# Performance work log

Hardware: AMD Instinct MI355X
Metric: run time of the kernel (lower is better)

The kernel has to match this reference:

```python
import jax, jax.numpy as jnp
import numpy as np

N_USERS, N_ITEMS = 100000, 50000
DIM = 128
E_U, E_I = 400000, 200000
B = 4096


def _init_layer(key, dim):
    k1, k2, k3 = jax.random.split(key, 3)
    s = 1.0 / np.sqrt(dim)
    W = jax.random.uniform(k1, (dim, dim), jnp.float32, -s, s)
    a_src = jax.random.uniform(k2, (dim,), jnp.float32, -s, s)
    a_dst = jax.random.uniform(k3, (dim,), jnp.float32, -s, s)
    return W, a_src, a_dst


def setup_inputs() -> dict:
    key = jax.random.key(0)
    ks = jax.random.split(key, 12)
    inp = {
        "uedg_index": jax.random.randint(ks[0], (2, E_U), 0, N_USERS),
        "iedg_index": jax.random.randint(ks[1], (2, E_I), 0, N_ITEMS),
        "user_id": jax.random.randint(ks[2], (B,), 0, N_USERS),
        "item_id": jax.random.randint(ks[3], (B,), 0, N_ITEMS),
        "uedg_value": jax.random.uniform(ks[4], (E_U,), jnp.float32),
        "iedg_value": jax.random.uniform(ks[5], (E_I,), jnp.float32),
        # learned parameters (t.rand init in the original)
        "user_matrix": jax.random.uniform(ks[6], (N_USERS, DIM), jnp.float32),
        "item_matrix": jax.random.uniform(ks[7], (N_ITEMS, DIM), jnp.float32),
    }
    for name, k in (("u1", ks[8]), ("u2", ks[9]), ("i1", ks[10]), ("i2", ks[11])):
        W, a_s, a_d = _init_layer(k, DIM)
        inp[f"W_{name}"] = W
        inp[f"a_src_{name}"] = a_s
        inp[f"a_dst_{name}"] = a_d
    return inp


def gat_layer(x, edge_index, edge_value, W, a_src, a_dst):
    """Single-head GAT layer with per-edge weights (dropout disabled / eval mode)."""
    n = x.shape[0]
    h = x @ W                                   # [N, D]
    src, dst = edge_index[0], edge_index[1]
    hs, hd = h[src], h[dst]                     # [E, D] gathers
    logits = jax.nn.leaky_relu((hs * a_src).sum(-1) + (hd * a_dst).sum(-1), 0.2)  # [E]
    # numerically-stable neighbor softmax over destination nodes
    m = jax.ops.segment_max(logits, dst, num_segments=n)
    e = jnp.exp(logits - m[dst]) * edge_value
    denom = jax.ops.segment_sum(e, dst, num_segments=n)
    coef = e / (denom[dst] + 1e-16)
    out = jax.ops.segment_sum(hs * coef[:, None], dst, num_segments=n)  # scatter-add aggregation
    return jax.nn.elu(out)


def reference(uedg_index, iedg_index, user_id, item_id, uedg_value, iedg_value,
              user_matrix, item_matrix,
              W_u1, a_src_u1, a_dst_u1, W_u2, a_src_u2, a_dst_u2,
              W_i1, a_src_i1, a_dst_i1, W_i2, a_src_i2, a_dst_i2):
    iout = gat_layer(item_matrix, iedg_index, iedg_value, W_i1, a_src_i1, a_dst_i1)
    uout = gat_layer(user_matrix, uedg_index, uedg_value, W_u1, a_src_u1, a_dst_u1)
    iout = gat_layer(iout, iedg_index, iedg_value, W_i2, a_src_i2, a_dst_i2)
    uout = gat_layer(uout, uedg_index, uedg_value, W_u2, a_src_u2, a_dst_u2)
    user_vc = uout[user_id]   # index_select over rows
    item_vc = iout[item_id]
    return user_vc, item_vc
```

## Files before the change

kernel.cpp:

```cpp
#include <hip/hip_runtime.h>
#include <hip/hip_bf16.h>

#define DIM 128
#define KSEG 32

typedef short bf16x8 __attribute__((ext_vector_type(8)));
typedef float f32x4  __attribute__((ext_vector_type(4)));

__device__ __forceinline__ float elu_f(float x) { return x > 0.f ? x : expm1f(x); }

__device__ __forceinline__ unsigned short f2bfu(float f) {
    return __builtin_bit_cast(unsigned short, __float2bfloat16(f));
}
__device__ __forceinline__ float bf2f(unsigned short b) {
    return __uint_as_float(((unsigned)b) << 16);
}

struct PrepArgs {
    const float* W[4];
    const float* as[4];
    const float* ad[4];
    unsigned short* Wt;
    unsigned short* wa;
};

__global__ __launch_bounds__(256) void init_all(int* __restrict__ z, int n, PrepArgs p, int nz)
{
    const int t = threadIdx.x;
    if ((int)blockIdx.x < nz) {
        int i = blockIdx.x * 256 + t;
        if (i < n) z[i] = 0;
        return;
    }
    __shared__ float as[DIM], ad[DIM];
    __shared__ float sr[4][2];
    const int pb    = blockIdx.x - nz;
    const int layer = pb >> 3;
    const int blk   = pb & 7;
    const float* W  = p.W[layer];
    unsigned short* W_t = p.Wt + layer * DIM * DIM;
    unsigned short* wa  = p.wa + layer * 2 * DIM;
    if (t < DIM) as[t] = p.as[layer][t];
    else ad[t - DIM] = p.ad[layer][t - DIM];
    __syncthreads();
    const int half = t >> 7;
    const int c = t & 127;
    const int wv = t >> 6;
    const int k_end = blk * 16 + 16;
    for (int k0 = blk * 16; k0 < k_end; k0 += 2) {
        const int k = k0 + half;
        float w = W[k * DIM + c];
        W_t[c * DIM + k] = f2bfu(w);
        float vs = w * as[c], vd = w * ad[c];
#pragma unroll
        for (int o = 32; o > 0; o >>= 1) { vs += __shfl_down(vs, o); vd += __shfl_down(vd, o); }
        if ((t & 63) == 0) { sr[wv][0] = vs; sr[wv][1] = vd; }
        __syncthreads();
        if (t < 2) {
            const int kk = k0 + t;
            wa[kk]       = f2bfu(sr[2 * t][0] + sr[2 * t + 1][0]);
            wa[DIM + kk] = f2bfu(sr[2 * t][1] + sr[2 * t + 1][1]);
        }
        __syncthreads();
    }
}

__global__ __launch_bounds__(256) void hist_gemm(
    const int* __restrict__ ued, const int* __restrict__ ied,
    const float* __restrict__ uval, const float* __restrict__ ival,
    int EU, int EI, int* __restrict__ cnt, int2* __restrict__ epair, int gH,
    const float* __restrict__ xu, const float* __restrict__ xi,
    const unsigned short* __restrict__ Wt_u, const unsigned short* __restrict__ Wt_i,
    const unsigned short* __restrict__ wa_u, const unsigned short* __restrict__ wa_i,
    unsigned short* __restrict__ h, float* __restrict__ s_src, float* __restrict__ s_dst,
    int NU, int NI, int gu)
{
    __shared__ short xs[2][64 * 128];
    const int t = threadIdx.x;

    if ((int)blockIdx.x < gH) {
        const int ET = EU + EI;
        const int stride = gH * 256;
        int e0 = blockIdx.x * 256 + t;
        int nd[4], sv[4]; float vv[4];
#pragma unroll
        for (int j = 0; j < 4; ++j) {
            int e = e0 + j * stride;
            nd[j] = -1;
            if (e < ET) {
                if (e < EU) { nd[j] = ued[EU + e]; sv[j] = ued[e]; vv[j] = uval[e]; }
                else { int ee = e - EU; nd[j] = NU + ied[EI + ee]; sv[j] = NU + ied[ee]; vv[j] = ival[ee]; }
            }
        }
        int rk[4];
#pragma unroll
        for (int j = 0; j < 4; ++j)
            if (nd[j] >= 0) rk[j] = atomicAdd(&cnt[nd[j]], 1);
#pragma unroll
        for (int j = 0; j < 4; ++j)
            if (nd[j] >= 0 && rk[j] < KSEG)
                epair[(size_t)nd[j] * KSEG + rk[j]] = make_int2(sv[j], __float_as_int(vv[j]));
        return;
    }

    const int wv = t >> 6;
    const int l  = t & 63;
    const int lo = l & 15;
    const int hi = l >> 4;

    const int gbid = blockIdx.x - gH;
    const bool isU = gbid < gu;
    const int b0   = isU ? gbid : gbid - gu;
    const int nblk = isU ? gu : (gridDim.x - gH - gu);
    const int Nl   = isU ? NU : NI;
    const int gofs = isU ? 0 : NU;
    const float* xf = isU ? xu : xi;
    const unsigned short* W_t = isU ? Wt_u : Wt_i;
    const unsigned short* wa  = isU ? wa_u : wa_i;
    const int ntiles = (Nl + 63) >> 6;
    if (b0 >= ntiles) return;

    bf16x8 wf[4][2];
#pragma unroll
    for (int cb2 = 0; cb2 < 2; ++cb2) {
        const unsigned short* base = W_t + (wv * 32 + cb2 * 16 + lo) * DIM + hi * 8;
#pragma unroll
        for (int kb = 0; kb < 4; ++kb)
            wf[kb][cb2] = *reinterpret_cast<const bf16x8*>(base + kb * 32);
    }
    bf16x8 sfrag[4];
    if (lo < 2) {
        const unsigned short* sb = wa + lo * DIM + hi * 8;
#pragma unroll
        for (int kb = 0; kb < 4; ++kb)
            sfrag[kb] = *reinterpret_cast<const bf16x8*>(sb + kb * 32);
    } else {
#pragma unroll
        for (int kb = 0; kb < 4; ++kb) {
            bf16x8 z = { 0, 0, 0, 0, 0, 0, 0, 0 };
            sfrag[kb] = z;
        }
    }

    int srow[4], suc[4];
#pragma unroll
    for (int i = 0; i < 4; ++i) {
        int unit = i * 256 + t;
        srow[i] = unit >> 4;
        suc[i]  = unit & 15;
    }
    float4 va[4], vb[4];

    auto LOADREGS = [&](int r0) {
#pragma unroll
        for (int i = 0; i < 4; ++i) {
            int gr = r0 + srow[i];
            if (gr < Nl) {
                const float4* p = reinterpret_cast<const float4*>(&xf[(size_t)gr * DIM + suc[i] * 8]);
                va[i] = p[0];
                vb[i] = p[1];
            } else {
                va[i] = make_float4(0.f, 0.f, 0.f, 0.f);
                vb[i] = make_float4(0.f, 0.f, 0.f, 0.f);
            }
        }
    };
    auto STORELDS = [&](int buf) {
#pragma unroll
        for (int i = 0; i < 4; ++i) {
            bf16x8 bv;
            bv[0] = (short)f2bfu(va[i].x); bv[1] = (short)f2bfu(va[i].y);
            bv[2] = (short)f2bfu(va[i].z); bv[3] = (short)f2bfu(va[i].w);
            bv[4] = (short)f2bfu(vb[i].x); bv[5] = (short)f2bfu(vb[i].y);
            bv[6] = (short)f2bfu(vb[i].z); bv[7] = (short)f2bfu(vb[i].w);
            int byte = srow[i] * 256 + ((suc[i] * 16) ^ ((srow[i] & 7) << 4));
            *reinterpret_cast<bf16x8*>(reinterpret_cast<char*>(xs[buf]) + byte) = bv;
        }
    };

    int tile = b0;
    LOADREGS(tile * 64);
    STORELDS(0);
    __syncthreads();
    int cur = 0;
    for (;;) {
        const int nextTile = tile + nblk;
        const bool more = nextTile < ntiles;
        if (more) LOADREGS(nextTile * 64);

        const int r0 = tile * 64;
#pragma unroll
        for (int rb = 0; rb < 4; ++rb) {
            const int arow = rb * 16 + lo;
            bf16x8 a[4];
#pragma unroll
            for (int kb = 0; kb < 4; ++kb) {
                int byte = arow * 256 + ((kb * 64 + hi * 16) ^ ((arow & 7) << 4));
                a[kb] = *reinterpret_cast<const bf16x8*>(reinterpret_cast<const char*>(xs[cur]) + byte);
            }
            f32x4 acc0 = {0.f,0.f,0.f,0.f}, acc1 = {0.f,0.f,0.f,0.f};
#pragma unroll
            for (int kb = 0; kb < 4; ++kb) {
                acc0 = __builtin_amdgcn_mfma_f32_16x16x32_bf16(a[kb], wf[kb][0], acc0, 0, 0, 0);
                acc1 = __builtin_amdgcn_mfma_f32_16x16x32_bf16(a[kb], wf[kb][1], acc1, 0, 0, 0);
            }
#pragma unroll
            for (int i = 0; i < 4; ++i) {
                int row = r0 + rb * 16 + hi * 4 + i;
                if (row < Nl) {
                    size_t grow = (size_t)(gofs + row);
                    h[grow * DIM + wv * 32 + lo]      = f2bfu(acc0[i]);
                    h[grow * DIM + wv * 32 + 16 + lo] = f2bfu(acc1[i]);
                }
            }
            if (rb == wv) {
                f32x4 acc_s = {0.f,0.f,0.f,0.f};
#pragma unroll
                for (int kb = 0; kb < 4; ++kb)
                    acc_s = __builtin_amdgcn_mfma_f32_16x16x32_bf16(a[kb], sfrag[kb], acc_s, 0, 0, 0);
#pragma unroll
                for (int i = 0; i < 4; ++i) {
                    int row = r0 + wv * 16 + hi * 4 + i;
                    if (row < Nl) {
                        if (lo == 0) s_src[gofs + row] = acc_s[i];
                        else if (lo == 1) s_dst[gofs + row] = acc_s[i];
                    }
                }
            }
        }

        if (!more) break;
        STORELDS(cur ^ 1);
        __syncthreads();
        cur ^= 1;
        tile = nextTile;
    }
}

__global__ __launch_bounds__(256) void mark_flag(const int* __restrict__ uid, const int* __restrict__ iid,
                                                 int B, int NU, const int* __restrict__ cnt,
                                                 const int2* __restrict__ epair, int* __restrict__ flag)
{
    int ent = (blockIdx.x * 256 + threadIdx.x) >> 4;
    int l16 = threadIdx.x & 15;
    if (ent >= 2 * B) return;
    int n = (ent < B) ? uid[ent] : NU + iid[ent - B];
    if (l16 == 0) flag[n] = 1;
    int md = min(cnt[n], KSEG);
    for (int e = l16; e < md; e += 16)
        flag[epair[(size_t)n * KSEG + e].x] = 1;
}

__global__ __launch_bounds__(256) void scan_partial(const int* __restrict__ cnt, int N, int* __restrict__ aux)
{
    __shared__ int sm[4];
    int i = blockIdx.x * 256 + threadIdx.x;
    int v = (i < N) ? cnt[i] : 0;
#pragma unroll
    for (int o = 32; o > 0; o >>= 1) v += __shfl_down(v, o);
    if ((threadIdx.x & 63) == 0) sm[threadIdx.x >> 6] = v;
    __syncthreads();
    if (threadIdx.x == 0) aux[blockIdx.x] = sm[0] + sm[1] + sm[2] + sm[3];
}

__global__ __launch_bounds__(1024) void scan_aux(int* __restrict__ aux, int nb)
{
    __shared__ int s[1024];
    int t = threadIdx.x;
    int v = (t < nb) ? aux[t] : 0;
    s[t] = v;
    __syncthreads();
    for (int o = 1; o < 1024; o <<= 1) {
        int u = (t >= o) ? s[t - o] : 0;
        __syncthreads();
        s[t] += u;
        __syncthreads();
    }
    if (t < nb) aux[t] = t ? s[t - 1] : 0;
}

__global__ __launch_bounds__(256) void scan_write(const int* __restrict__ cnt, const int* __restrict__ aux,
                                                  int N, int* __restrict__ rowptr)
{
    __shared__ int s[256];
    int t = threadIdx.x;
    int i = blockIdx.x * 256 + t;
    int v = (i < N) ? cnt[i] : 0;
    s[t] = v;
    __syncthreads();
    for (int o = 1; o < 256; o <<= 1) {
        int u = (t >= o) ? s[t - o] : 0;
        __syncthreads();
        s[t] += u;
        __syncthreads();
    }
    int excl = aux[blockIdx.x] + s[t] - v;
    if (i < N) rowptr[i] = excl;
    if (i == N - 1) rowptr[N] = excl + v;
}

__global__ __launch_bounds__(256) void build_alist(const int* __restrict__ flag, const int* __restrict__ cidx,
                                                   int NT, int NU, int* __restrict__ alist, int* __restrict__ cpos)
{
    int i = blockIdx.x * 256 + threadIdx.x;
    const int nau = cidx[NU], na = cidx[NT];
    const int nau_pad = (nau + 63) & ~63;
    const int nap = nau_pad + (na - nau);
    if (i < NT && flag[i]) {
        int pos = (i < NU) ? cidx[i] : nau_pad + (cidx[i] - nau);
        alist[pos] = i;
        cpos[i] = pos;
    }
    if (i < 64) {
        int s = nau + i;
        if (s < nau_pad) alist[s] = -1;
    } else if (i < 128) {
        alist[nap + (i - 64)] = -1;
    }
}

__global__ __launch_bounds__(256) void csr_agg_act(const int* __restrict__ cnt, const int2* __restrict__ epair,
                                                   const float* __restrict__ ssrc, const float* __restrict__ sdst,
                                                   const unsigned short* __restrict__ h,
                                                   unsigned short* __restrict__ outb,
                                                   const int* __restrict__ alist, const int* __restrict__ cidx,
                                                   int NU, int NT)
{
    const int nau = cidx[NU], na = cidx[NT];
    const int nap = ((nau + 63) & ~63) + (na - nau);
    int g = (blockIdx.x * 256 + threadIdx.x) >> 4;
    int l16 = threadIdx.x & 15;
    if (g >= nap) return;
    int n = alist[g];
    if (n < 0) return;
    const size_t beg = (size_t)n * KSEG;
    int md = min(cnt[n], KSEG);
    float sd = sdst[n];
    float m = -INFINITY, den = 0.f;
    float acc[8] = {0,0,0,0,0,0,0,0};
    for (int base = 0; base < md; base += 16) {
        int c16 = min(16, md - base);
        int sidx = 0; float l = -INFINITY, evv = 0.f;
        if (l16 < c16) {
            int2 pr = epair[beg + base + l16];
            sidx = pr.x;
            evv = __int_as_float(pr.y);
            float ll = ssrc[sidx] + sd;
            l = ll >= 0.f ? ll : 0.2f * ll;
        }
        float cm = l;
#pragma unroll
        for (int o = 8; o > 0; o >>= 1) cm = fmaxf(cm, __shfl_xor(cm, o, 16));
        float nm = fmaxf(m, cm);
        float sc = __expf(m - nm);
        den *= sc;
#pragma unroll
        for (int j = 0; j < 8; ++j) acc[j] *= sc;
        float p = (l16 < c16) ? __expf(l - nm) * evv : 0.f;
        float ps = p;
#pragma unroll
        for (int o = 8; o > 0; o >>= 1) ps += __shfl_xor(ps, o, 16);
        den += ps;
        for (int k0 = 0; k0 < c16; k0 += 4) {
            bf16x8 hv[4]; float cc[4];
#pragma unroll
            for (int j = 0; j < 4; ++j) {
                int k = k0 + j;
                cc[j] = 0.f;
                if (k < c16) {
                    cc[j] = __shfl(p, k, 16);
                    int s = __shfl(sidx, k, 16);
                    hv[j] = *reinterpret_cast<const bf16x8*>(&h[(size_t)s * DIM + l16 * 8]);
                }
            }
#pragma unroll
            for (int j = 0; j < 4; ++j) {
                if (k0 + j < c16) {
#pragma unroll
                    for (int q = 0; q < 8; ++q)
                        acc[q] = fmaf(bf2f((unsigned short)hv[j][q]), cc[j], acc[q]);
                }
            }
        }
        m = nm;
    }
    float inv = 1.f / (den + 1e-16f);
    bf16x8 o;
#pragma unroll
    for (int q = 0; q < 8; ++q) o[q] = (short)f2bfu(elu_f(acc[q] * inv));
    *reinterpret_cast<bf16x8*>(&outb[(size_t)n * DIM + l16 * 8]) = o;
}

__global__ __launch_bounds__(256) void gemm_act(const unsigned short* __restrict__ xbb,
                                                const unsigned short* __restrict__ Wt_u,
                                                const unsigned short* __restrict__ Wt_i,
                                                const unsigned short* __restrict__ wa_u,
                                                const unsigned short* __restrict__ wa_i,
                                                unsigned short* __restrict__ h, float* __restrict__ s_src,
                                                float* __restrict__ s_dst,
                                                const int* __restrict__ alist, const int* __restrict__ cidx,
                                                int NU, int NT)
{
    const int nau = cidx[NU], na = cidx[NT];
    const int nau_pad = (nau + 63) & ~63;
    const int nap = nau_pad + (na - nau);
    const int r0 = blockIdx.x * 64;
    if (r0 >= nap) return;

    __shared__ short xs[64 * 128];
    __shared__ int rowid[64];
    const int t  = threadIdx.x;
    const int wv = t >> 6;
    const int l  = t & 63;
    const int lo = l & 15;
    const int hi = l >> 4;

    const bool isU = r0 < nau_pad;
    const unsigned short* W_t = isU ? Wt_u : Wt_i;
    const unsigned short* wa  = isU ? wa_u : wa_i;

    if (t < 64) rowid[t] = alist[r0 + t];
    __syncthreads();

    bf16x8 wf[4][2];
#pragma unroll
    for (int cb2 = 0; cb2 < 2; ++cb2) {
        const unsigned short* base = W_t + (wv * 32 + cb2 * 16 + lo) * DIM + hi * 8;
#pragma unroll
        for (int kb = 0; kb < 4; ++kb)
            wf[kb][cb2] = *reinterpret_cast<const bf16x8*>(base + kb * 32);
    }
    bf16x8 sfrag[4];
    if (lo < 2) {
        const unsigned short* sb = wa + lo * DIM + hi * 8;
#pragma unroll
        for (int kb = 0; kb < 4; ++kb)
            sfrag[kb] = *reinterpret_cast<const bf16x8*>(sb + kb * 32);
    } else {
#pragma unroll
        for (int kb = 0; kb < 4; ++kb) {
            bf16x8 z = { 0, 0, 0, 0, 0, 0, 0, 0 };
            sfrag[kb] = z;
        }
    }

#pragma unroll
    for (int i = 0; i < 4; ++i) {
        int unit = i * 256 + t;
        int row = unit >> 4, uc = unit & 15;
        int node = rowid[row];
        bf16x8 bv = { 0, 0, 0, 0, 0, 0, 0, 0 };
        if (node >= 0)
            bv = *reinterpret_cast<const bf16x8*>(&xbb[(size_t)node * DIM + uc * 8]);
        int byte = row * 256 + ((uc * 16) ^ ((row & 7) << 4));
        *reinterpret_cast<bf16x8*>(reinterpret_cast<char*>(xs) + byte) = bv;
    }
    __syncthreads();

#pragma unroll
    for (int rb = 0; rb < 4; ++rb) {
        const int arow = rb * 16 + lo;
        bf16x8 a[4];
#pragma unroll
        for (int kb = 0; kb < 4; ++kb) {
            int byte = arow * 256 + ((kb * 64 + hi * 16) ^ ((arow & 7) << 4));
            a[kb] = *reinterpret_cast<const bf16x8*>(reinterpret_cast<const char*>(xs) + byte);
        }
        f32x4 acc0 = {0.f,0.f,0.f,0.f}, acc1 = {0.f,0.f,0.f,0.f};
#pragma unroll
        for (int kb = 0; kb < 4; ++kb) {
            acc0 = __builtin_amdgcn_mfma_f32_16x16x32_bf16(a[kb], wf[kb][0], acc0, 0, 0, 0);
            acc1 = __builtin_amdgcn_mfma_f32_16x16x32_bf16(a[kb], wf[kb][1], acc1, 0, 0, 0);
        }
#pragma unroll
        for (int i = 0; i < 4; ++i) {
            int row = rb * 16 + hi * 4 + i;
            if (rowid[row] >= 0) {
                size_t grow = (size_t)(r0 + row);
                h[grow * DIM + wv * 32 + lo]      = f2bfu(acc0[i]);
                h[grow * DIM + wv * 32 + 16 + lo] = f2bfu(acc1[i]);
            }
        }
        if (rb == wv) {
            f32x4 acc_s = {0.f,0.f,0.f,0.f};
#pragma unroll
            for (int kb = 0; kb < 4; ++kb)
                acc_s = __builtin_amdgcn_mfma_f32_16x16x32_bf16(a[kb], sfrag[kb], acc_s, 0, 0, 0);
#pragma unroll
            for (int i = 0; i < 4; ++i) {
                int row = wv * 16 + hi * 4 + i;
                if (rowid[row] >= 0) {
                    if (lo == 0) s_src[r0 + row] = acc_s[i];
                    else if (lo == 1) s_dst[r0 + row] = acc_s[i];
                }
            }
        }
    }
}

__global__ __launch_bounds__(256) void csr_agg_batch(const int* __restrict__ cnt, const int2* __restrict__ epair,
                                                     const float* __restrict__ ssrc, const float* __restrict__ sdst,
                                                     const unsigned short* __restrict__ h,
                                                     const int* __restrict__ cpos,
                                                     const int* __restrict__ uid, const int* __restrict__ iid,
                                                     float* __restrict__ out, int B, int NU)
{
    int ent = (blockIdx.x * 256 + threadIdx.x) >> 4;
    int l16 = threadIdx.x & 15;
    if (ent >= 2 * B) return;
    int n = (ent < B) ? uid[ent] : NU + iid[ent - B];
    const size_t beg = (size_t)n * KSEG;
    int md = min(cnt[n], KSEG);
    float sd = sdst[cpos[n]];
    float m = -INFINITY, den = 0.f;
    float acc[8] = {0,0,0,0,0,0,0,0};
    for (int base = 0; base < md; base += 16) {
        int c16 = min(16, md - base);
        int cps = 0; float l = -INFINITY, evv = 0.f;
        if (l16 < c16) {
            int2 pr = epair[beg + base + l16];
            cps = cpos[pr.x];
            evv = __int_as_float(pr.y);
            float ll = ssrc[cps] + sd;
            l = ll >= 0.f ? ll : 0.2f * ll;
        }
        float cm = l;
#pragma unroll
        for (int o = 8; o > 0; o >>= 1) cm = fmaxf(cm, __shfl_xor(cm, o, 16));
        float nm = fmaxf(m, cm);
        float sc = __expf(m - nm);
        den *= sc;
#pragma unroll
        for (int j = 0; j < 8; ++j) acc[j] *= sc;
        float p = (l16 < c16) ? __expf(l - nm) * evv : 0.f;
        float ps = p;
#pragma unroll
        for (int o = 8; o > 0; o >>= 1) ps += __shfl_xor(ps, o, 16);
        den += ps;
        for (int k0 = 0; k0 < c16; k0 += 4) {
            bf16x8 hv[4]; float cc[4];
#pragma unroll
            for (int j = 0; j < 4; ++j) {
                int k = k0 + j;
                cc[j] = 0.f;
                if (k < c16) {
                    cc[j] = __shfl(p, k, 16);
                    int s = __shfl(cps, k, 16);
                    hv[j] = *reinterpret_cast<const bf16x8*>(&h[(size_t)s * DIM + l16 * 8]);
                }
            }
#pragma unroll
            for (int j = 0; j < 4; ++j) {
                if (k0 + j < c16) {
#pragma unroll
                    for (int q = 0; q < 8; ++q)
                        acc[q] = fmaf(bf2f((unsigned short)hv[j][q]), cc[j], acc[q]);
                }
            }
        }
        m = nm;
    }
    float inv = 1.f / (den + 1e-16f);
    float4 o0 = { elu_f(acc[0]*inv), elu_f(acc[1]*inv), elu_f(acc[2]*inv), elu_f(acc[3]*inv) };
    float4 o1 = { elu_f(acc[4]*inv), elu_f(acc[5]*inv), elu_f(acc[6]*inv), elu_f(acc[7]*inv) };
    float4* op = reinterpret_cast<float4*>(&out[(size_t)ent * DIM + l16 * 8]);
    op[0] = o0;
    op[1] = o1;
}

extern "C" void kernel_launch(void* const* d_in, const int* in_sizes, int n_in,
                              void* d_out, int out_size, void* d_ws, size_t ws_size,
                              hipStream_t stream)
{
    const int*   uedg    = (const int*)d_in[0];
    const int*   iedg    = (const int*)d_in[1];
    const int*   user_id = (const int*)d_in[2];
    const int*   item_id = (const int*)d_in[3];
    const float* uval    = (const float*)d_in[4];
    const float* ival    = (const float*)d_in[5];
    const float* umat    = (const float*)d_in[6];
    const float* imat    = (const float*)d_in[7];
    const float* W_u1 = (const float*)d_in[8];
    const float* as_u1 = (const float*)d_in[9];
    const float* ad_u1 = (const float*)d_in[10];
    const float* W_u2 = (const float*)d_in[11];
    const float* as_u2 = (const float*)d_in[12];
    const float* ad_u2 = (const float*)d_in[13];
    const float* W_i1 = (const float*)d_in[14];
    const float* as_i1 = (const float*)d_in[15];
    const float* ad_i1 = (const float*)d_in[16];
    const float* W_i2 = (const float*)d_in[17];
    const float* as_i2 = (const float*)d_in[18];
    const float* ad_i2 = (const float*)d_in[19];

    const int EU = in_sizes[0] / 2;
    const int EI = in_sizes[1] / 2;
    const int B  = in_sizes[2];
    const int NU = in_sizes[6] / DIM;
    const int NI = in_sizes[7] / DIM;
    const int NT = NU + NI;
    const int ET = EU + EI;
    const int nb = (NT + 255) / 256;

    unsigned short* h    = (unsigned short*)d_ws;
    unsigned short* Wt_a = h + (size_t)NT * DIM;
    unsigned short* wa_a = Wt_a + 4 * DIM * DIM;
    unsigned short* xbb  = wa_a + 4 * 2 * DIM;
    float* ssrc   = (float*)(xbb + (size_t)NT * DIM);
    float* sdst   = ssrc + NT;
    int2*  epair  = (int2*)(sdst + NT);
    int*   cnt    = (int*)(epair + (size_t)NT * KSEG);
    int*   flag   = cnt + NT;
    int*   cidx   = flag + NT;
    int*   aux    = cidx + (NT + 1);
    int*   alist  = aux + 1024;
    int*   cpos   = alist + (NT + 128);

    PrepArgs pa;
    pa.W[0] = W_u1; pa.W[1] = W_u2; pa.W[2] = W_i1; pa.W[3] = W_i2;
    pa.as[0] = as_u1; pa.as[1] = as_u2; pa.as[2] = as_i1; pa.as[3] = as_i2;
    pa.ad[0] = ad_u1; pa.ad[1] = ad_u2; pa.ad[2] = ad_i1; pa.ad[3] = ad_i2;
    pa.Wt = Wt_a; pa.wa = wa_a;

    const int zn = 2 * NT;
    const int nz = (zn + 255) / 256;
    init_all<<<nz + 32, 256, 0, stream>>>(cnt, zn, pa, nz);

    const int gH = (ET + 1023) / 1024;
    const int gu = 512, gi = 256;
    hist_gemm<<<gH + gu + gi, 256, 0, stream>>>(
        uedg, iedg, uval, ival, EU, EI, cnt, epair, gH,
        umat, imat, Wt_a + 0 * DIM * DIM, Wt_a + 2 * DIM * DIM,
        wa_a + 0 * 2 * DIM, wa_a + 2 * 2 * DIM, h, ssrc, sdst, NU, NI, gu);

    mark_flag<<<(2 * B * 16 + 255) / 256, 256, 0, stream>>>(user_id, item_id, B, NU, cnt, epair, flag);

    scan_partial<<<nb, 256, 0, stream>>>(flag, NT, aux);
    scan_aux<<<1, 1024, 0, stream>>>(aux, nb);
    scan_write<<<nb, 256, 0, stream>>>(flag, aux, NT, cidx);
    build_alist<<<(NT + 255) / 256, 256, 0, stream>>>(flag, cidx, NT, NU, alist, cpos);

    csr_agg_act<<<(NT + 128 + 15) / 16, 256, 0, stream>>>(cnt, epair, ssrc, sdst, h, xbb, alist, cidx, NU, NT);

    gemm_act<<<(NT + 192) / 64, 256, 0, stream>>>(xbb,
        Wt_a + 1 * DIM * DIM, Wt_a + 3 * DIM * DIM, wa_a + 1 * 2 * DIM, wa_a + 3 * 2 * DIM,
        h, ssrc, sdst, alist, cidx, NU, NT);

    csr_agg_batch<<<(2 * B * 16 + 255) / 256, 256, 0, stream>>>(cnt, epair, ssrc, sdst, h, cpos,
        user_id, item_id, (float*)d_out, B, NU);
}
```

Baseline: 112.3 us.

## Build CSR edge lists only for batch nodes and their neighbours

```diff
diff --git a/kernel.cpp b/kernel.cpp
--- a/kernel.cpp
+++ b/kernel.cpp
@@ -65,10 +65,21 @@
     }
 }
 
-__global__ __launch_bounds__(256) void hist_gemm(
+__global__ __launch_bounds__(256) void mark_isB(const int* __restrict__ uid, const int* __restrict__ iid,
+                                                int B, int NU, int* __restrict__ isB, int* __restrict__ flag)
+{
+    int ent = blockIdx.x * 256 + threadIdx.x;
+    if (ent >= 2 * B) return;
+    int n = (ent < B) ? uid[ent] : NU + iid[ent - B];
+    isB[n] = 1;
+    flag[n] = 1;
+}
+
+__global__ __launch_bounds__(256) void pass1_gemm(
     const int* __restrict__ ued, const int* __restrict__ ied,
     const float* __restrict__ uval, const float* __restrict__ ival,
-    int EU, int EI, int* __restrict__ cnt, int2* __restrict__ epair, int gH,
+    int EU, int EI, const int* __restrict__ isB, int* __restrict__ flag,
+    int* __restrict__ cnt, int2* __restrict__ epair, int gH,
     const float* __restrict__ xu, const float* __restrict__ xi,
     const unsigned short* __restrict__ Wt_u, const unsigned short* __restrict__ Wt_i,
     const unsigned short* __restrict__ wa_u, const unsigned short* __restrict__ wa_i,
@@ -82,7 +93,7 @@
         const int ET = EU + EI;
         const int stride = gH * 256;
         int e0 = blockIdx.x * 256 + t;
-        int nd[4], sv[4]; float vv[4];
+        int nd[4], sv[4]; float vv[4]; int ib[4];
 #pragma unroll
         for (int j = 0; j < 4; ++j) {
             int e = e0 + j * stride;
@@ -92,14 +103,18 @@
                 else { int ee = e - EU; nd[j] = NU + ied[EI + ee]; sv[j] = NU + ied[ee]; vv[j] = ival[ee]; }
             }
         }
-        int rk[4];
 #pragma unroll
         for (int j = 0; j < 4; ++j)
-            if (nd[j] >= 0) rk[j] = atomicAdd(&cnt[nd[j]], 1);
-#pragma unroll
-        for (int j = 0; j < 4; ++j)
-            if (nd[j] >= 0 && rk[j] < KSEG)
-                epair[(size_t)nd[j] * KSEG + rk[j]] = make_int2(sv[j], __float_as_int(vv[j]));
+            ib[j] = (nd[j] >= 0) ? isB[nd[j]] : 0;
+#pragma unroll
+        for (int j = 0; j < 4; ++j) {
+            if (ib[j]) {
+                int rk = atomicAdd(&cnt[nd[j]], 1);
+                if (rk < KSEG)
+                    epair[(size_t)nd[j] * KSEG + rk] = make_int2(sv[j], __float_as_int(vv[j]));
+                flag[sv[j]] = 1;
+            }
+        }
         return;
     }
 
@@ -237,30 +252,49 @@
     }
 }
 
-__global__ __launch_bounds__(256) void mark_flag(const int* __restrict__ uid, const int* __restrict__ iid,
-                                                 int B, int NU, const int* __restrict__ cnt,
-                                                 const int2* __restrict__ epair, int* __restrict__ flag)
-{
-    int ent = (blockIdx.x * 256 + threadIdx.x) >> 4;
-    int l16 = threadIdx.x & 15;
-    if (ent >= 2 * B) return;
-    int n = (ent < B) ? uid[ent] : NU + iid[ent - B];
-    if (l16 == 0) flag[n] = 1;
-    int md = min(cnt[n], KSEG);
-    for (int e = l16; e < md; e += 16)
-        flag[epair[(size_t)n * KSEG + e].x] = 1;
-}
-
-__global__ __launch_bounds__(256) void scan_partial(const int* __restrict__ cnt, int N, int* __restrict__ aux)
-{
+__global__ __launch_bounds__(256) void pass2_scan(
+    const int* __restrict__ ued, const int* __restrict__ ied,
+    const float* __restrict__ uval, const float* __restrict__ ival,
+    int EU, int EI, const int* __restrict__ isB, const int* __restrict__ flag,
+    int* __restrict__ cnt, int2* __restrict__ epair, int gP,
+    int NT, int* __restrict__ aux, int NU)
+{
+    const int t = threadIdx.x;
+    if ((int)blockIdx.x < gP) {
+        const int ET = EU + EI;
+        const int stride = gP * 256;
+        int e0 = blockIdx.x * 256 + t;
+        int nd[4], sv[4]; float vv[4]; int act[4];
+#pragma unroll
+        for (int j = 0; j < 4; ++j) {
+            int e = e0 + j * stride;
+            nd[j] = -1;
+            if (e < ET) {
+                if (e < EU) { nd[j] = ued[EU + e]; sv[j] = ued[e]; vv[j] = uval[e]; }
+                else { int ee = e - EU; nd[j] = NU + ied[EI + ee]; sv[j] = NU + ied[ee]; vv[j] = ival[ee]; }
+            }
+        }
+#pragma unroll
+        for (int j = 0; j < 4; ++j)
+            act[j] = (nd[j] >= 0) ? (flag[nd[j]] && !isB[nd[j]]) : 0;
+#pragma unroll
+        for (int j = 0; j < 4; ++j) {
+            if (act[j]) {
+                int rk = atomicAdd(&cnt[nd[j]], 1);
+                if (rk < KSEG)
+                    epair[(size_t)nd[j] * KSEG + rk] = make_int2(sv[j], __float_as_int(vv[j]));
+            }
+        }
+        return;
+    }
     __shared__ int sm[4];
-    int i = blockIdx.x * 256 + threadIdx.x;
-    int v = (i < N) ? cnt[i] : 0;
+    int i = (blockIdx.x - gP) * 256 + t;
+    int v = (i < NT) ? flag[i] : 0;
 #pragma unroll
     for (int o = 32; o > 0; o >>= 1) v += __shfl_down(v, o);
-    if ((threadIdx.x & 63) == 0) sm[threadIdx.x >> 6] = v;
+    if ((t & 63) == 0) sm[t >> 6] = v;
     __syncthreads();
-    if (threadIdx.x == 0) aux[blockIdx.x] = sm[0] + sm[1] + sm[2] + sm[3];
+    if (t == 0) aux[blockIdx.x - gP] = sm[0] + sm[1] + sm[2] + sm[3];
 }
 
 __global__ __launch_bounds__(1024) void scan_aux(int* __restrict__ aux, int nb)
@@ -611,7 +645,8 @@
     int2*  epair  = (int2*)(sdst + NT);
     int*   cnt    = (int*)(epair + (size_t)NT * KSEG);
     int*   flag   = cnt + NT;
-    int*   cidx   = flag + NT;
+    int*   isB    = flag + NT;
+    int*   cidx   = isB + NT;
     int*   aux    = cidx + (NT + 1);
     int*   alist  = aux + 1024;
     int*   cpos   = alist + (NT + 128);
@@ -622,20 +657,23 @@
     pa.ad[0] = ad_u1; pa.ad[1] = ad_u2; pa.ad[2] = ad_i1; pa.ad[3] = ad_i2;
     pa.Wt = Wt_a; pa.wa = wa_a;
 
-    const int zn = 2 * NT;
+    const int zn = 3 * NT;
     const int nz = (zn + 255) / 256;
     init_all<<<nz + 32, 256, 0, stream>>>(cnt, zn, pa, nz);
 
+    mark_isB<<<(2 * B + 255) / 256, 256, 0, stream>>>(user_id, item_id, B, NU, isB, flag);
+
     const int gH = (ET + 1023) / 1024;
     const int gu = 512, gi = 256;
-    hist_gemm<<<gH + gu + gi, 256, 0, stream>>>(
-        uedg, iedg, uval, ival, EU, EI, cnt, epair, gH,
+    pass1_gemm<<<gH + gu + gi, 256, 0, stream>>>(
+        uedg, iedg, uval, ival, EU, EI, isB, flag, cnt, epair, gH,
         umat, imat, Wt_a + 0 * DIM * DIM, Wt_a + 2 * DIM * DIM,
         wa_a + 0 * 2 * DIM, wa_a + 2 * 2 * DIM, h, ssrc, sdst, NU, NI, gu);
 
-    mark_flag<<<(2 * B * 16 + 255) / 256, 256, 0, stream>>>(user_id, item_id, B, NU, cnt, epair, flag);
-
-    scan_partial<<<nb, 256, 0, stream>>>(flag, NT, aux);
+    const int gP = (ET + 1023) / 1024;
+    pass2_scan<<<gP + nb, 256, 0, stream>>>(uedg, iedg, uval, ival, EU, EI, isB, flag, cnt, epair, gP,
+                                            NT, aux, NU);
+
     scan_aux<<<1, 1024, 0, stream>>>(aux, nb);
     scan_write<<<nb, 256, 0, stream>>>(flag, aux, NT, cidx);
     build_alist<<<(NT + 255) / 256, 256, 0, stream>>>(flag, cidx, NT, NU, alist, cpos);
```

Result: faster. 96.70 us (-13.9%).
